# Optimization experiments

Measured on AMD Instinct MI355X. Metric: run time of the kernel, lower is better.

Reference implementation:

```python
import jax, jax.numpy as jnp
import numpy as np

B, L, D, H, F, NL, K, G = 2, 2048, 768, 12, 3072, 12, 128, 16
HD = D // H
SCALE = HD ** -0.5


def setup_inputs() -> dict:
    key = jax.random.key(0)
    ks = jax.random.split(key, 8)
    n = lambda k, s, std=0.02: jax.random.normal(k, s, dtype=jnp.float32) * std
    return {
        "x": jax.random.normal(ks[0], (B, L, D), dtype=jnp.float32),
        "pos_conv_w": n(ks[1], (D, D // G, K)),
        "pos_conv_b": jnp.zeros((D,), jnp.float32),
        "ln0_g": jnp.ones((D,), jnp.float32), "ln0_b": jnp.zeros((D,), jnp.float32),
        "Wq": n(ks[2], (NL, D, D)), "bq": jnp.zeros((NL, D), jnp.float32),
        "Wk": n(ks[3], (NL, D, D)), "bk": jnp.zeros((NL, D), jnp.float32),
        "Wv": n(ks[4], (NL, D, D)), "bv": jnp.zeros((NL, D), jnp.float32),
        "Wo": n(ks[5], (NL, D, D)), "bo": jnp.zeros((NL, D), jnp.float32),
        "ln1_g": jnp.ones((NL, D), jnp.float32), "ln1_b": jnp.zeros((NL, D), jnp.float32),
        "W1": n(ks[6], (NL, D, F)), "b1": jnp.zeros((NL, F), jnp.float32),
        "W2": n(ks[7], (NL, F, D)), "b2": jnp.zeros((NL, D), jnp.float32),
        "ln2_g": jnp.ones((NL, D), jnp.float32), "ln2_b": jnp.zeros((NL, D), jnp.float32),
    }


def _ln(x, g, b, eps=1e-5):
    m = jnp.mean(x, axis=-1, keepdims=True)
    v = jnp.mean(jnp.square(x - m), axis=-1, keepdims=True)
    return (x - m) * jax.lax.rsqrt(v + eps) * g + b


def reference(x, pos_conv_w, pos_conv_b, ln0_g, ln0_b, Wq, bq, Wk, bk, Wv, bv, Wo, bo,
              ln1_g, ln1_b, W1, b1, W2, b2, ln2_g, ln2_b):
    b_, l_, d_ = x.shape
    # positional grouped conv embedding (kernel even -> drop last frame), GELU, residual add
    pos = jax.lax.conv_general_dilated(x.transpose(0, 2, 1), pos_conv_w, (1,), [(K // 2, K // 2)],
                                       feature_group_count=G)  # (B, D, L+1)
    pos = pos[:, :, :l_] + pos_conv_b[None, :, None]
    h = x + jax.nn.gelu(pos, approximate=False).transpose(0, 2, 1)
    # post-norm encoder (layer_norm_first=False): LN applied before the layer stack
    h = _ln(h, ln0_g, ln0_b)

    def layer(h, p):
        wq, bq_, wk, bk_, wv, bv_, wo, bo_, g1, be1, w1, bf1, w2, bf2, g2, be2 = p
        r = h
        q = (h @ wq + bq_).reshape(b_, l_, H, HD)
        k = (h @ wk + bk_).reshape(b_, l_, H, HD)
        v = (h @ wv + bv_).reshape(b_, l_, H, HD)
        w = jax.nn.softmax(SCALE * jnp.einsum('blhd,bmhd->bhlm', q, k), axis=-1)
        o = jnp.einsum('bhlm,bmhd->blhd', w, v).reshape(b_, l_, d_)
        h = r + (o @ wo + bo_)
        h = _ln(h, g1, be1)
        ff = jax.nn.gelu(h @ w1 + bf1, approximate=False) @ w2 + bf2
        h = _ln(h + ff, g2, be2)
        return h, None

    h, _ = jax.lax.scan(layer, h, (Wq, bq, Wk, bk, Wv, bv, Wo, bo,
                                   ln1_g, ln1_b, W1, b1, W2, b2, ln2_g, ln2_b))
    return h
```

## Files before the change

kernel.cpp:

```cpp
#include <hip/hip_runtime.h>
#include <hip/hip_bf16.h>
#include <stdint.h>

#define B_ 2
#define L_ 2048
#define D_ 768
#define H_ 12
#define F_ 3072
#define NL_ 12
#define K_ 128
#define G_ 16
#define HD_ 64
#define CPG_ 48
#define M_TOK (B_*L_)
#define SCALE_ 0.125f

typedef __hip_bfloat16 bf16;
typedef __bf16 bf16x8 __attribute__((ext_vector_type(8)));
typedef float f32x4 __attribute__((ext_vector_type(4)));

__device__ __forceinline__ void gload16(const void* g, void* l) {
  __builtin_amdgcn_global_load_lds((const __attribute__((address_space(1))) void*)g,
                                   (__attribute__((address_space(3))) void*)l, 16, 0, 0);
}

__global__ __launch_bounds__(256) void convw_kernel(const float* __restrict__ w,
                                                    bf16* __restrict__ wT2) {
  int idx = blockIdx.x * 256 + threadIdx.x;
  int ci = idx & 63;
  int row = idx >> 6;
  int d = row % 48;
  int t2 = row / 48;
  int kk = t2 & 127;
  int g = t2 >> 7;
  float v = (ci < 48) ? w[(((size_t)(g * 48 + d) * 48) + ci) * 128 + kk] : 0.f;
  wT2[idx] = __float2bfloat16(v);
}

__global__ __launch_bounds__(256) void conv_mfma(const float* __restrict__ x,
                                                 const bf16* __restrict__ wT2,
                                                 const float* __restrict__ bias,
                                                 float* __restrict__ out) {
  int flat = blockIdx.x;
  int wgid = (flat & 7) * 64 + (flat >> 3);
  const int g = wgid >> 5;
  int rem = wgid & 31;
  const int l0 = (rem & 15) * 128;
  const int b = rem >> 4;

  const int tid = threadIdx.x, w = tid >> 6, lane = tid & 63;
  const int c15 = lane & 15, g4 = lane >> 4;
  __shared__ __align__(16) bf16 win[256 * 64];
  __shared__ __align__(16) bf16 Wl[2][2 * 48 * 64];

  {
    int lg = l0 - 64 + tid;
    char* dst = (char*)win + tid * 128;
    int swr = (tid & 7) << 4;
    uint4 z4 = {0u, 0u, 0u, 0u};
    if ((unsigned)lg < 2048u) {
      const float* srow = x + ((size_t)(b * 2048 + lg) * 768 + g * 48);
#pragma unroll
      for (int c = 0; c < 6; ++c) {
        float4 v0 = *(const float4*)(srow + c * 8);
        float4 v1 = *(const float4*)(srow + c * 8 + 4);
        union { bf16 h[8]; uint4 u; } uu;
        uu.h[0] = __float2bfloat16(v0.x); uu.h[1] = __float2bfloat16(v0.y);
        uu.h[2] = __float2bfloat16(v0.z); uu.h[3] = __float2bfloat16(v0.w);
        uu.h[4] = __float2bfloat16(v1.x); uu.h[5] = __float2bfloat16(v1.y);
        uu.h[6] = __float2bfloat16(v1.z); uu.h[7] = __float2bfloat16(v1.w);
        *(uint4*)(dst + ((c * 16) ^ swr)) = uu.u;
      }
    } else {
#pragma unroll
      for (int c = 0; c < 6; ++c) *(uint4*)(dst + ((c * 16) ^ swr)) = z4;
    }
    *(uint4*)(dst + (96 ^ swr)) = z4;
    *(uint4*)(dst + (112 ^ swr)) = z4;
  }

  const char* wbase = (const char*)wT2 + (size_t)g * 128 * 48 * 128;

  const int coff = w * 3072;
#define STAGEW(kp, bufi)                                                                   \
  {                                                                                        \
    _Pragma("unroll")                                                                      \
    for (int i = 0; i < 3; ++i) {                                                          \
      int c = coff + i * 1024 + (lane << 4);                                               \
      int row96 = c >> 7;                                                                  \
      int s = row96 / 48;                                                                  \
      int d = row96 - s * 48;                                                              \
      int cb2 = c & 127;                                                                   \
      gload16(wbase + ((size_t)((2 * (kp) + s) * 48 + d)) * 128 + (cb2 ^ ((d & 7) << 4)),  \
              (char*)Wl[bufi] + coff + i * 1024);                                          \
    }                                                                                      \
  }

  f32x4 acc[2][3];
  const f32x4 vzero = {0.f, 0.f, 0.f, 0.f};
#pragma unroll
  for (int i = 0; i < 2; ++i)
#pragma unroll
    for (int j = 0; j < 3; ++j) acc[i][j] = vzero;

  STAGEW(0, 0);
  __syncthreads();

  for (int kp = 0; kp < 64; ++kp) {
    int cur = kp & 1;
    if (kp + 1 < 64) STAGEW(kp + 1, cur ^ 1);
    const char* Wc = (const char*)Wl[cur];
#pragma unroll
    for (int s = 0; s < 2; ++s) {
      int kk = 2 * kp + s;
#pragma unroll
      for (int cb = 0; cb < 2; ++cb) {
        int a0r = w * 16 + c15 + kk;
        int a1r = 64 + a0r;
        bf16x8 a0 = *(const bf16x8*)((const char*)win + a0r * 128 + ((cb * 64 + g4 * 16) ^ ((a0r & 7) << 4)));
        bf16x8 a1 = *(const bf16x8*)((const char*)win + a1r * 128 + ((cb * 64 + g4 * 16) ^ ((a1r & 7) << 4)));
#pragma unroll
        for (int ct = 0; ct < 3; ++ct) {
          int d = ct * 16 + c15;
          bf16x8 bfrag = *(const bf16x8*)(Wc + s * 6144 + d * 128 +
                                          ((cb * 64 + g4 * 16) ^ ((d & 7) << 4)));
          acc[0][ct] = __builtin_amdgcn_mfma_f32_16x16x32_bf16(a0, bfrag, acc[0][ct], 0, 0, 0);
          acc[1][ct] = __builtin_amdgcn_mfma_f32_16x16x32_bf16(a1, bfrag, acc[1][ct], 0, 0, 0);
        }
      }
    }
    __syncthreads();
  }
#undef STAGEW

#pragma unroll
  for (int ls = 0; ls < 2; ++ls)
#pragma unroll
    for (int ct = 0; ct < 3; ++ct) {
      int dg = g * 48 + ct * 16 + c15;
      float bv = bias[dg];
#pragma unroll
      for (int r = 0; r < 4; ++r) {
        int l = l0 + ls * 64 + w * 16 + g4 * 4 + r;
        size_t idx = (size_t)(b * 2048 + l) * 768 + dg;
        float vv = acc[ls][ct][r] + bv;
        vv = 0.5f * vv * (1.0f + erff(vv * 0.70710678f));
        out[idx] = x[idx] + vv;
      }
    }
}

__global__ __launch_bounds__(256) void ln_kernel(const float* __restrict__ a,
                                                 const float* __restrict__ g,
                                                 const float* __restrict__ be,
                                                 bf16* __restrict__ outb) {
  int w = threadIdx.x >> 6, lane = threadIdx.x & 63;
  size_t row = (size_t)blockIdx.x * 4 + w;
  const float* ar = a + row * 768;
  float4 v[3];
  float s = 0.f;
#pragma unroll
  for (int i = 0; i < 3; ++i) {
    int c = lane * 4 + i * 256;
    float4 vv = *(const float4*)(ar + c);
    v[i] = vv;
    s += vv.x + vv.y + vv.z + vv.w;
  }
#pragma unroll
  for (int st = 1; st < 64; st <<= 1) s += __shfl_xor(s, st);
  float mean = s * (1.0f / 768.0f);
  float s2 = 0.f;
#pragma unroll
  for (int i = 0; i < 3; ++i) {
    float dx = v[i].x - mean, dy = v[i].y - mean, dz = v[i].z - mean, dw = v[i].w - mean;
    s2 += dx * dx + dy * dy + dz * dz + dw * dw;
  }
#pragma unroll
  for (int st = 1; st < 64; st <<= 1) s2 += __shfl_xor(s2, st);
  float rstd = rsqrtf(s2 * (1.0f / 768.0f) + 1e-5f);
#pragma unroll
  for (int i = 0; i < 3; ++i) {
    int c = lane * 4 + i * 256;
    float4 gv = *(const float4*)(g + c);
    float4 bv = *(const float4*)(be + c);
    union { bf16 h[4]; uint2 u; } pk;
    pk.h[0] = __float2bfloat16((v[i].x - mean) * rstd * gv.x + bv.x);
    pk.h[1] = __float2bfloat16((v[i].y - mean) * rstd * gv.y + bv.y);
    pk.h[2] = __float2bfloat16((v[i].z - mean) * rstd * gv.z + bv.z);
    pk.h[3] = __float2bfloat16((v[i].w - mean) * rstd * gv.w + bv.w);
    *(uint2*)(outb + row * 768 + c) = pk.u;
  }
}

template <int F32OUT>
__global__ __launch_bounds__(256) void ln_bf(const bf16* __restrict__ a,
                                             const bf16* __restrict__ r,
                                             const float* __restrict__ g,
                                             const float* __restrict__ be,
                                             bf16* __restrict__ outb,
                                             float* __restrict__ outf) {
  int w = threadIdx.x >> 6, lane = threadIdx.x & 63;
  size_t row = (size_t)blockIdx.x * 4 + w;
  const bf16* ar = a + row * 768;
  const bf16* rr = r + row * 768;
  float v[3][4];
  float s = 0.f;
#pragma unroll
  for (int i = 0; i < 3; ++i) {
    int c = lane * 4 + i * 256;
    union { uint2 u; uint16_t h[4]; } ua, urr;
    ua.u = *(const uint2*)(ar + c);
    urr.u = *(const uint2*)(rr + c);
#pragma unroll
    for (int j = 0; j < 4; ++j) {
      float x = __uint_as_float((uint32_t)ua.h[j] << 16) +
                __uint_as_float((uint32_t)urr.h[j] << 16);
      v[i][j] = x; s += x;
    }
  }
#pragma unroll
  for (int st = 1; st < 64; st <<= 1) s += __shfl_xor(s, st);
  float mean = s * (1.0f / 768.0f);
  float s2 = 0.f;
#pragma unroll
  for (int i = 0; i < 3; ++i)
#pragma unroll
    for (int j = 0; j < 4; ++j) {
      float d2 = v[i][j] - mean;
      s2 += d2 * d2;
    }
#pragma unroll
  for (int st = 1; st < 64; st <<= 1) s2 += __shfl_xor(s2, st);
  float rstd = rsqrtf(s2 * (1.0f / 768.0f) + 1e-5f);
#pragma unroll
  for (int i = 0; i < 3; ++i) {
    int c = lane * 4 + i * 256;
    float4 gv = *(const float4*)(g + c);
    float4 bv = *(const float4*)(be + c);
    float o0 = (v[i][0] - mean) * rstd * gv.x + bv.x;
    float o1 = (v[i][1] - mean) * rstd * gv.y + bv.y;
    float o2 = (v[i][2] - mean) * rstd * gv.z + bv.z;
    float o3 = (v[i][3] - mean) * rstd * gv.w + bv.w;
    union { bf16 h[4]; uint2 u; } pk;
    pk.h[0] = __float2bfloat16(o0); pk.h[1] = __float2bfloat16(o1);
    pk.h[2] = __float2bfloat16(o2); pk.h[3] = __float2bfloat16(o3);
    *(uint2*)(outb + row * 768 + c) = pk.u;
    if (F32OUT) {
      float4 of = {o0, o1, o2, o3};
      *(float4*)(outf + row * 768 + c) = of;
    }
  }
}

__global__ __launch_bounds__(256) void prep_weights(const float* __restrict__ WqB,
                                                    const float* __restrict__ WkB,
                                                    const float* __restrict__ WvB,
                                                    const float* __restrict__ WoB,
                                                    const float* __restrict__ W1B,
                                                    const float* __restrict__ W2B,
                                                    const float* __restrict__ bqB,
                                                    const float* __restrict__ bkB,
                                                    const float* __restrict__ bvB,
                                                    bf16* __restrict__ wqkvb,
                                                    bf16* __restrict__ wob,
                                                    bf16* __restrict__ w1b,
                                                    bf16* __restrict__ w2b,
                                                    float* __restrict__ bqkv,
                                                    int l) {
  __shared__ float t[32][33];
  int tid = threadIdx.x;
  int tx = tid & 31, ty = tid >> 5;
  const float* wq = WqB + (size_t)l * 768 * 768;
  const float* wk = WkB + (size_t)l * 768 * 768;
  const float* wv = WvB + (size_t)l * 768 * 768;
  const float* wo = WoB + (size_t)l * 768 * 768;
  const float* w1 = W1B + (size_t)l * 768 * 3072;
  const float* w2 = W2B + (size_t)l * 3072 * 768;

  int blk = blockIdx.x;
  if (blk >= 6912) {
    int i = (blk - 6912) * 256 + tid;
    if (i < 2304)
      bqkv[i] = (i < 768) ? bqB[(size_t)l * 768 + i]
              : (i < 1536) ? bkB[(size_t)l * 768 + i - 768]
                           : bvB[(size_t)l * 768 + i - 1536];
    return;
  }
  if (blk < 1728) {
    int n0 = (blk % 72) * 32, k0 = (blk / 72) * 32;
    const float* src = (n0 < 768) ? wq : (n0 < 1536) ? wk : wv;
    int nn = (n0 >= 1536) ? (n0 - 1536) : (n0 >= 768 ? n0 - 768 : n0);
#pragma unroll
    for (int i = 0; i < 32; i += 8) t[ty + i][tx] = src[(size_t)(k0 + ty + i) * 768 + nn + tx];
    __syncthreads();
#pragma unroll
    for (int i = 0; i < 32; i += 8)
      wqkvb[(size_t)(n0 + ty + i) * 768 + k0 + tx] = __float2bfloat16(t[tx][ty + i]);
    return;
  }
  blk -= 1728;
  if (blk < 576) {
    int c0 = (blk % 24) * 32, r0 = (blk / 24) * 32;
#pragma unroll
    for (int i = 0; i < 32; i += 8) t[ty + i][tx] = wo[(size_t)(r0 + ty + i) * 768 + c0 + tx];
    __syncthreads();
#pragma unroll
    for (int i = 0; i < 32; i += 8)
      wob[(size_t)(c0 + ty + i) * 768 + r0 + tx] = __float2bfloat16(t[tx][ty + i]);
    return;
  }
  blk -= 576;
  if (blk < 2304) {
    int c0 = (blk % 96) * 32, r0 = (blk / 96) * 32;
#pragma unroll
    for (int i = 0; i < 32; i += 8) t[ty + i][tx] = w1[(size_t)(r0 + ty + i) * 3072 + c0 + tx];
    __syncthreads();
#pragma unroll
    for (int i = 0; i < 32; i += 8)
      w1b[(size_t)(c0 + ty + i) * 768 + r0 + tx] = __float2bfloat16(t[tx][ty + i]);
    return;
  }
  blk -= 2304;
  {
    int c0 = (blk % 24) * 32, r0 = (blk / 24) * 32;
#pragma unroll
    for (int i = 0; i < 32; i += 8) t[ty + i][tx] = w2[(size_t)(r0 + ty + i) * 768 + c0 + tx];
    __syncthreads();
#pragma unroll
    for (int i = 0; i < 32; i += 8)
      w2b[(size_t)(c0 + ty + i) * 3072 + r0 + tx] = __float2bfloat16(t[tx][ty + i]);
  }
}

template <int BM, int BN, int BK, int GELU, int BF16OUT, int VOUT = 0>
__global__ __launch_bounds__(256) void gemm_bf16(const bf16* __restrict__ A,
                                                 const bf16* __restrict__ BT,
                                                 const float* __restrict__ bias,
                                                 void* __restrict__ Cout,
                                                 int N, int Kd,
                                                 bf16* __restrict__ vTout = nullptr) {
  constexpr int WM = BM / 2, MF = WM / 16;
  constexpr int WN = BN / 2, FN = WN / 16;
  constexpr int KF = BK / 32;
  constexpr int ROWB = BK * 2;
  constexpr int RPC = 1024 / ROWB;
  constexpr int NCH = BM * BK / 512;
  __shared__ bf16 As[BM * BK];
  __shared__ bf16 Bs[BN * BK];
  const int tid = threadIdx.x, w = tid >> 6, lane = tid & 63;
  int gx = gridDim.x;
  int flat = blockIdx.x + gx * blockIdx.y;
  int cpx = (gx * gridDim.y) >> 3;
  int sw = (flat & 7) * cpx + (flat >> 3);
  const int bn = sw % gx, bm = sw / gx;
  const int wr = w >> 1, wc = w & 1;
  const int c15 = lane & 15, g4 = lane >> 4;
  const int rowInC = lane / (ROWB / 16);
  const int colb = (lane % (ROWB / 16)) * 16;

  f32x4 acc[MF][FN];
  const f32x4 vzero = {0.f, 0.f, 0.f, 0.f};
#pragma unroll
  for (int i = 0; i < MF; ++i)
#pragma unroll
    for (int j = 0; j < FN; ++j) acc[i][j] = vzero;

  const char* Ab = (const char*)A;
  const char* Bb = (const char*)BT;

  for (int k0 = 0; k0 < Kd; k0 += BK) {
#pragma unroll
    for (int i = 0; i < NCH / 4; ++i) {
      int t = w + 4 * i;
      int row = t * RPC + rowInC;
      gload16(Ab + ((size_t)(bm * BM + row) * Kd + k0) * 2 + (colb ^ ((row & 7) << 4)),
              (char*)As + t * 1024);
    }
#pragma unroll
    for (int i = 0; i < (BN * BK / 512) / 4; ++i) {
      int t = w + 4 * i;
      int row = t * RPC + rowInC;
      gload16(Bb + ((size_t)(bn * BN + row) * Kd + k0) * 2 + (colb ^ ((row & 7) << 4)),
              (char*)Bs + t * 1024);
    }
    __syncthreads();
    bf16x8 af[MF][KF], bfr[FN][KF];
#pragma unroll
    for (int kf = 0; kf < KF; ++kf) {
      int kbyte = kf * 64 + g4 * 16;
#pragma unroll
      for (int mf = 0; mf < MF; ++mf) {
        int row = wr * WM + mf * 16 + c15;
        af[mf][kf] = *(const bf16x8*)((const char*)As + row * ROWB + (kbyte ^ ((row & 7) << 4)));
      }
#pragma unroll
      for (int fn = 0; fn < FN; ++fn) {
        int row = wc * WN + fn * 16 + c15;
        bfr[fn][kf] = *(const bf16x8*)((const char*)Bs + row * ROWB + (kbyte ^ ((row & 7) << 4)));
      }
    }
    __builtin_amdgcn_s_setprio(1);
#pragma unroll
    for (int mf = 0; mf < MF; ++mf)
#pragma unroll
      for (int fn = 0; fn < FN; ++fn)
#pragma unroll
        for (int kf = 0; kf < KF; ++kf)
          acc[mf][fn] = __builtin_amdgcn_mfma_f32_16x16x32_bf16(af[mf][kf], bfr[fn][kf], acc[mf][fn], 0, 0, 0);
    __builtin_amdgcn_s_setprio(0);
    __syncthreads();
  }
#pragma unroll
  for (int fn = 0; fn < FN; ++fn) {
    int col = bn * BN + wc * WN + fn * 16 + c15;
    float bv = bias[col];
#pragma unroll
    for (int mf = 0; mf < MF; ++mf) {
#pragma unroll
      for (int r = 0; r < 4; ++r) {
        int row = bm * BM + wr * WM + mf * 16 + g4 * 4 + r;
        float vv = acc[mf][fn][r] + bv;
        if (GELU) vv = 0.5f * vv * (1.0f + erff(vv * 0.70710678f));
        if (BF16OUT) {
          if (VOUT && col >= 1536) {
            int hd2 = col - 1536, hh = hd2 >> 6, dd = hd2 & 63;
            int bb = row >> 11, ll = row & 2047;
            vTout[((size_t)((bb * 12 + hh) * 64 + dd) << 11) + ll] = __float2bfloat16(vv);
          } else {
            ((bf16*)Cout)[(size_t)row * N + col] = __float2bfloat16(vv);
          }
        } else {
          ((float*)Cout)[(size_t)row * N + col] = vv;
        }
      }
    }
  }
}

__global__ __launch_bounds__(256) void attn_mfma(const bf16* __restrict__ qkv,
                                                 const bf16* __restrict__ vT,
                                                 bf16* __restrict__ ob) {
  int bid = blockIdx.x + 32 * (blockIdx.y + 12 * blockIdx.z);
  int wgid = (bid & 7) * 96 + (bid >> 3);
  const int q0 = (wgid & 31) * 64;
  int bh = wgid >> 5;
  const int h = bh % 12, b = bh / 12;

  const int tid = threadIdx.x, w = tid >> 6, lane = tid & 63;
  const int c15 = lane & 15, g4 = lane >> 4;
  const int lrow8 = lane >> 3;
  const int cb = (lane & 7) * 16;
  __shared__ bf16 Kl[2][4096];
  __shared__ bf16 Vl[2][4096];
  __shared__ bf16 Pl[4096];

  const f32x4 vzero = {0.f, 0.f, 0.f, 0.f};
  const char* qp = (const char*)qkv + (((size_t)(b * 2048 + q0 + w * 16 + c15)) * 2304 + h * 64) * 2;
  bf16x8 qa0 = *(const bf16x8*)(qp + g4 * 16);
  bf16x8 qa1 = *(const bf16x8*)(qp + 64 + g4 * 16);

  bf16x8 b_one;
#pragma unroll
  for (int i = 0; i < 8; ++i) b_one[i] = (__bf16)1.0f;

  f32x4 o[4], o5;
#pragma unroll
  for (int i = 0; i < 4; ++i) o[i] = vzero;
  o5 = vzero;
  float m = -1e30f;
  const float SC2 = 0.18033688f;
  const float THR = 11.54f;

  const char* kgb = (const char*)qkv + (((size_t)(b * 2048)) * 2304 + 768 + h * 64) * 2;
  const char* vgb = (const char*)vT + ((size_t)((b * 12 + h) * 64) * 2048) * 2;
  char* Plw = (char*)Pl + w * 2048;

  const int rr0 = w * 8 + lrow8;
  const int swz = cb ^ (lrow8 << 4);
  const char* ka0 = kgb + (size_t)rr0 * 4608 + swz;
  const char* ka1 = ka0 + 32 * 4608;
  const char* va0 = vgb + (size_t)rr0 * 4096 + swz;
  const char* va1 = va0 + 32 * 4096;
  char* kd0 = (char*)Kl[0] + w * 1024;
  char* vd0 = (char*)Vl[0] + w * 1024;

#define STAGE(kt, bufi)                                                        \
  {                                                                            \
    size_t ko = (size_t)(kt) * 294912;                                         \
    size_t vo = (size_t)(kt) * 128;                                            \
    int lo = (bufi) * 8192;                                                    \
    gload16(ka0 + ko, kd0 + lo);                                               \
    gload16(ka1 + ko, kd0 + lo + 4096);                                        \
    gload16(va0 + vo, vd0 + lo);                                               \
    gload16(va1 + vo, vd0 + lo + 4096);                                        \
  }

  STAGE(0, 0);
  __syncthreads();

  for (int kt = 0; kt < 32; ++kt) {
    int cur = kt & 1;
    if (kt + 1 < 32) STAGE(kt + 1, cur ^ 1);

    const char* Kc = (const char*)Kl[cur];
    const char* Vc = (const char*)Vl[cur];

    f32x4 sc[4];
    __builtin_amdgcn_s_setprio(1);
#pragma unroll
    for (int fn = 0; fn < 4; ++fn) {
      int key = fn * 16 + c15;
      const char* kr = Kc + key * 128;
      int sw = (key & 7) << 4;
      bf16x8 kb0 = *(const bf16x8*)(kr + ((g4 * 16) ^ sw));
      bf16x8 kb1 = *(const bf16x8*)(kr + ((64 + g4 * 16) ^ sw));
      f32x4 s = __builtin_amdgcn_mfma_f32_16x16x32_bf16(kb0, qa0, vzero, 0, 0, 0);
      s = __builtin_amdgcn_mfma_f32_16x16x32_bf16(kb1, qa1, s, 0, 0, 0);
      sc[fn] = s;
    }
    __builtin_amdgcn_s_setprio(0);

    float pm = fmaxf(
        fmaxf(fmaxf(fmaxf(sc[0][0], sc[0][1]), fmaxf(sc[0][2], sc[0][3])),
              fmaxf(fmaxf(sc[1][0], sc[1][1]), fmaxf(sc[1][2], sc[1][3]))),
        fmaxf(fmaxf(fmaxf(sc[2][0], sc[2][1]), fmaxf(sc[2][2], sc[2][3])),
              fmaxf(fmaxf(sc[3][0], sc[3][1]), fmaxf(sc[3][2], sc[3][3]))));
    int ok = (pm * SC2 <= m + THR) ? 1 : 0;

    if (!__all(ok)) {
      float tm = pm;
      tm = fmaxf(tm, __shfl_xor(tm, 16));
      tm = fmaxf(tm, __shfl_xor(tm, 32));
      float mn = fmaxf(m, tm * SC2);
      float alpha = exp2f(m - mn);
      m = mn;
#pragma unroll
      for (int r = 0; r < 4; ++r) {
        float ar = __shfl(alpha, g4 * 4 + r);
        o[0][r] *= ar; o[1][r] *= ar; o[2][r] *= ar; o[3][r] *= ar;
        o5[r] *= ar;
      }
    }

    {
      char* prow = Plw + c15 * 128;
      int swp = (c15 & 7) << 4;
#pragma unroll
      for (int fn = 0; fn < 4; ++fn) {
        union { bf16 hh[4]; uint2 u; } pk;
#pragma unroll
        for (int r = 0; r < 4; ++r)
          pk.hh[r] = __float2bfloat16(exp2f(fmaf(sc[fn][r], SC2, -m)));
        *(uint2*)(prow + ((fn * 32 + g4 * 8) ^ swp)) = pk.u;
      }
    }

    {
      const char* pr = Plw + c15 * 128;
      int sw = (c15 & 7) << 4;
      bf16x8 pa0 = *(const bf16x8*)(pr + ((g4 * 16) ^ sw));
      bf16x8 pa1 = *(const bf16x8*)(pr + ((64 + g4 * 16) ^ sw));
      __builtin_amdgcn_s_setprio(1);
#pragma unroll
      for (int fh = 0; fh < 4; ++fh) {
        int hd = fh * 16 + c15;
        const char* vr = Vc + hd * 128;
        int swv = (hd & 7) << 4;
        bf16x8 vb0 = *(const bf16x8*)(vr + ((g4 * 16) ^ swv));
        bf16x8 vb1 = *(const bf16x8*)(vr + ((64 + g4 * 16) ^ swv));
        o[fh] = __builtin_amdgcn_mfma_f32_16x16x32_bf16(pa0, vb0, o[fh], 0, 0, 0);
        o[fh] = __builtin_amdgcn_mfma_f32_16x16x32_bf16(pa1, vb1, o[fh], 0, 0, 0);
      }
      o5 = __builtin_amdgcn_mfma_f32_16x16x32_bf16(pa0, b_one, o5, 0, 0, 0);
      o5 = __builtin_amdgcn_mfma_f32_16x16x32_bf16(pa1, b_one, o5, 0, 0, 0);
      __builtin_amdgcn_s_setprio(0);
    }
    __syncthreads();
  }
#undef STAGE

#pragma unroll
  for (int r = 0; r < 4; ++r) {
    float inv = 1.0f / o5[r];
    size_t row = (size_t)(b * 2048 + q0 + w * 16 + g4 * 4 + r);
#pragma unroll
    for (int fh = 0; fh < 4; ++fh)
      ob[row * 768 + h * 64 + fh * 16 + c15] = __float2bfloat16(o[fh][r] * inv);
  }
}

extern "C" void kernel_launch(void* const* d_in, const int* in_sizes, int n_in,
                              void* d_out, int out_size, void* d_ws, size_t ws_size,
                              hipStream_t stream) {
  const float* x      = (const float*)d_in[0];
  const float* pcw    = (const float*)d_in[1];
  const float* pcb    = (const float*)d_in[2];
  const float* ln0_g  = (const float*)d_in[3];
  const float* ln0_b  = (const float*)d_in[4];
  const float* Wq     = (const float*)d_in[5];
  const float* bq     = (const float*)d_in[6];
  const float* Wk     = (const float*)d_in[7];
  const float* bk     = (const float*)d_in[8];
  const float* Wv     = (const float*)d_in[9];
  const float* bv     = (const float*)d_in[10];
  const float* Wo     = (const float*)d_in[11];
  const float* bo     = (const float*)d_in[12];
  const float* ln1_g  = (const float*)d_in[13];
  const float* ln1_b  = (const float*)d_in[14];
  const float* W1     = (const float*)d_in[15];
  const float* b1     = (const float*)d_in[16];
  const float* W2     = (const float*)d_in[17];
  const float* b2     = (const float*)d_in[18];
  const float* ln2_g  = (const float*)d_in[19];
  const float* ln2_b  = (const float*)d_in[20];

  const size_t MDB = (size_t)M_TOK * D_ * 4;
  char* W = (char*)d_ws;
  float* tmp  = (float*)(W + MDB);
  char*  big  = W + 2 * MDB;
  bf16*  qkv  = (bf16*)big;
  bf16*  ff   = (bf16*)big;
  bf16*  wT2  = (bf16*)big;
  bf16*  tmp_bf = (bf16*)W;
  char* p = W + 2 * MDB + 25165824;
  bf16* h_bf  = (bf16*)p; p += (size_t)M_TOK * D_ * 2;
  bf16* obuf  = (bf16*)p; p += (size_t)M_TOK * D_ * 2;
  bf16* vT    = (bf16*)p; p += (size_t)M_TOK * D_ * 2;
  bf16* wqkvb = (bf16*)p; p += (size_t)2304 * 768 * 2;
  bf16* wob   = (bf16*)p; p += (size_t)768 * 768 * 2;
  bf16* w1b   = (bf16*)p; p += (size_t)3072 * 768 * 2;
  bf16* w2b   = (bf16*)p; p += (size_t)768 * 3072 * 2;
  float* bqkv = (float*)p;

  convw_kernel<<<24576, 256, 0, stream>>>(pcw, wT2);
  conv_mfma<<<512, 256, 0, stream>>>(x, wT2, pcb, tmp);
  ln_kernel<<<M_TOK / 4, 256, 0, stream>>>(tmp, ln0_g, ln0_b, h_bf);

  for (int l = 0; l < NL_; ++l) {
    prep_weights<<<6921, 256, 0, stream>>>(Wq, Wk, Wv, Wo, W1, W2, bq, bk, bv,
                                           wqkvb, wob, w1b, w2b, bqkv, l);

    gemm_bf16<128, 128, 64, 0, 1, 1><<<dim3(18, 32), 256, 0, stream>>>(h_bf, wqkvb, bqkv, qkv, 2304, 768, vT);
    attn_mfma<<<dim3(32, 12, 2), 256, 0, stream>>>(qkv, vT, obuf);
    gemm_bf16<64, 64, 128, 0, 1><<<dim3(12, 64), 256, 0, stream>>>(obuf, wob, bo + (size_t)l * D_, tmp_bf, 768, 768);
    ln_bf<0><<<M_TOK / 4, 256, 0, stream>>>(tmp_bf, h_bf, ln1_g + (size_t)l * D_, ln1_b + (size_t)l * D_, h_bf, nullptr);
    gemm_bf16<128, 128, 64, 1, 1><<<dim3(24, 32), 256, 0, stream>>>(h_bf, w1b, b1 + (size_t)l * F_, ff, 3072, 768);
    gemm_bf16<64, 64, 128, 0, 1><<<dim3(12, 64), 256, 0, stream>>>(ff, w2b, b2 + (size_t)l * D_, tmp_bf, 768, 3072);
    if (l == NL_ - 1)
      ln_bf<1><<<M_TOK / 4, 256, 0, stream>>>(tmp_bf, h_bf, ln2_g + (size_t)l * D_, ln2_b + (size_t)l * D_, h_bf, (float*)d_out);
    else
      ln_bf<0><<<M_TOK / 4, 256, 0, stream>>>(tmp_bf, h_bf, ln2_g + (size_t)l * D_, ln2_b + (size_t)l * D_, h_bf, nullptr);
  }
}
```

Measured before the change: 2.256 ms.

## Software-pipeline attention: compute next QK tile before current softmax and PV

Restructures the flash-attention main loop so the QK^T MFMAs for tile kt+1 are issued before the softmax and PV work for tile kt, using two score register sets. K and V loads are split and prefetched two tiles ahead, with V moved to a triple-buffered LDS array. The goal is to overlap MFMA work with the exp/max softmax math and with global-to-LDS load latency. The cost is more register pressure and LDS, which could lower occupancy. The barrier-driven vmcnt waits may also limit how much overlap is actually achieved.

```diff
diff --git a/kernel.cpp b/kernel.cpp
--- a/kernel.cpp
+++ b/kernel.cpp
@@ -80,7 +80,6 @@
   }
 
   const char* wbase = (const char*)wT2 + (size_t)g * 128 * 48 * 128;
-
   const int coff = w * 3072;
 #define STAGEW(kp, bufi)                                                                   \
   {                                                                                        \
@@ -451,7 +450,7 @@
   const int lrow8 = lane >> 3;
   const int cb = (lane & 7) * 16;
   __shared__ bf16 Kl[2][4096];
-  __shared__ bf16 Vl[2][4096];
+  __shared__ bf16 Vl[3][4096];
   __shared__ bf16 Pl[4096];
 
   const f32x4 vzero = {0.f, 0.f, 0.f, 0.f};
@@ -484,100 +483,123 @@
   char* kd0 = (char*)Kl[0] + w * 1024;
   char* vd0 = (char*)Vl[0] + w * 1024;
 
-#define STAGE(kt, bufi)                                                        \
+#define STAGE_K(kt, bufi)                                                      \
   {                                                                            \
     size_t ko = (size_t)(kt) * 294912;                                         \
-    size_t vo = (size_t)(kt) * 128;                                            \
     int lo = (bufi) * 8192;                                                    \
     gload16(ka0 + ko, kd0 + lo);                                               \
     gload16(ka1 + ko, kd0 + lo + 4096);                                        \
+  }
+#define STAGE_V(kt, bufi)                                                      \
+  {                                                                            \
+    size_t vo = (size_t)(kt) * 128;                                            \
+    int lo = (bufi) * 8192;                                                    \
     gload16(va0 + vo, vd0 + lo);                                               \
     gload16(va1 + vo, vd0 + lo + 4096);                                        \
   }
 
-  STAGE(0, 0);
+#define DO_QK(SC, kbuf)                                                        \
+  {                                                                            \
+    const char* Kc = (const char*)Kl[kbuf];                                    \
+    __builtin_amdgcn_s_setprio(1);                                             \
+    _Pragma("unroll")                                                          \
+    for (int fn = 0; fn < 4; ++fn) {                                           \
+      int key = fn * 16 + c15;                                                 \
+      const char* kr = Kc + key * 128;                                         \
+      int swk = (key & 7) << 4;                                                \
+      bf16x8 kb0 = *(const bf16x8*)(kr + ((g4 * 16) ^ swk));                   \
+      bf16x8 kb1 = *(const bf16x8*)(kr + ((64 + g4 * 16) ^ swk));              \
+      f32x4 s = __builtin_amdgcn_mfma_f32_16x16x32_bf16(kb0, qa0, vzero, 0, 0, 0); \
+      s = __builtin_amdgcn_mfma_f32_16x16x32_bf16(kb1, qa1, s, 0, 0, 0);       \
+      SC[fn] = s;                                                              \
+    }                                                                          \
+    __builtin_amdgcn_s_setprio(0);                                             \
+  }
+
+#define DO_SMPV(SC, vbuf)                                                      \
+  {                                                                            \
+    float pm = fmaxf(                                                          \
+        fmaxf(fmaxf(fmaxf(SC[0][0], SC[0][1]), fmaxf(SC[0][2], SC[0][3])),     \
+              fmaxf(fmaxf(SC[1][0], SC[1][1]), fmaxf(SC[1][2], SC[1][3]))),    \
+        fmaxf(fmaxf(fmaxf(SC[2][0], SC[2][1]), fmaxf(SC[2][2], SC[2][3])),     \
+              fmaxf(fmaxf(SC[3][0], SC[3][1]), fmaxf(SC[3][2], SC[3][3]))));   \
+    int ok = (pm * SC2 <= m + THR) ? 1 : 0;                                    \
+    if (!__all(ok)) {                                                          \
+      float tm = pm;                                                           \
+      tm = fmaxf(tm, __shfl_xor(tm, 16));                                      \
+      tm = fmaxf(tm, __shfl_xor(tm, 32));                                      \
+      float mn = fmaxf(m, tm * SC2);                                           \
+      float alpha = exp2f(m - mn);                                             \
+      m = mn;                                                                  \
+      _Pragma("unroll")                                                        \
+      for (int r = 0; r < 4; ++r) {                                            \
+        float ar = __shfl(alpha, g4 * 4 + r);                                  \
+        o[0][r] *= ar; o[1][r] *= ar; o[2][r] *= ar; o[3][r] *= ar;            \
+        o5[r] *= ar;                                                           \
+      }                                                                        \
+    }                                                                          \
+    {                                                                          \
+      char* prow = Plw + c15 * 128;                                            \
+      int swp = (c15 & 7) << 4;                                                \
+      _Pragma("unroll")                                                        \
+      for (int fn = 0; fn < 4; ++fn) {                                         \
+        union { bf16 hh[4]; uint2 u; } pk;                                     \
+        _Pragma("unroll")                                                      \
+        for (int r = 0; r < 4; ++r)                                            \
+          pk.hh[r] = __float2bfloat16(exp2f(fmaf(SC[fn][r], SC2, -m)));        \
+        *(uint2*)(prow + ((fn * 32 + g4 * 8) ^ swp)) = pk.u;                   \
+      }                                                                        \
+    }                                                                          \
+    {                                                                          \
+      const char* pr = Plw + c15 * 128;                                        \
+      int swp2 = (c15 & 7) << 4;                                               \
+      bf16x8 pa0 = *(const bf16x8*)(pr + ((g4 * 16) ^ swp2));                  \
+      bf16x8 pa1 = *(const bf16x8*)(pr + ((64 + g4 * 16) ^ swp2));             \
+      const char* Vc = (const char*)Vl[vbuf];                                  \
+      __builtin_amdgcn_s_setprio(1);                                           \
+      _Pragma("unroll")                                                        \
+      for (int fh = 0; fh < 4; ++fh) {                                         \
+        int hd = fh * 16 + c15;                                                \
+        const char* vr = Vc + hd * 128;                                        \
+        int swv = (hd & 7) << 4;                                               \
+        bf16x8 vb0 = *(const bf16x8*)(vr + ((g4 * 16) ^ swv));                 \
+        bf16x8 vb1 = *(const bf16x8*)(vr + ((64 + g4 * 16) ^ swv));            \
+        o[fh] = __builtin_amdgcn_mfma_f32_16x16x32_bf16(pa0, vb0, o[fh], 0, 0, 0); \
+        o[fh] = __builtin_amdgcn_mfma_f32_16x16x32_bf16(pa1, vb1, o[fh], 0, 0, 0); \
+      }                                                                        \
+      o5 = __builtin_amdgcn_mfma_f32_16x16x32_bf16(pa0, b_one, o5, 0, 0, 0);   \
+      o5 = __builtin_amdgcn_mfma_f32_16x16x32_bf16(pa1, b_one, o5, 0, 0, 0);   \
+      __builtin_amdgcn_s_setprio(0);                                           \
+    }                                                                          \
+  }
+
+  STAGE_K(0, 0); STAGE_K(1, 1); STAGE_V(0, 0); STAGE_V(1, 1);
   __syncthreads();
 
-  for (int kt = 0; kt < 32; ++kt) {
-    int cur = kt & 1;
-    if (kt + 1 < 32) STAGE(kt + 1, cur ^ 1);
-
-    const char* Kc = (const char*)Kl[cur];
-    const char* Vc = (const char*)Vl[cur];
-
-    f32x4 sc[4];
-    __builtin_amdgcn_s_setprio(1);
-#pragma unroll
-    for (int fn = 0; fn < 4; ++fn) {
-      int key = fn * 16 + c15;
-      const char* kr = Kc + key * 128;
-      int sw = (key & 7) << 4;
-      bf16x8 kb0 = *(const bf16x8*)(kr + ((g4 * 16) ^ sw));
-      bf16x8 kb1 = *(const bf16x8*)(kr + ((64 + g4 * 16) ^ sw));
-      f32x4 s = __builtin_amdgcn_mfma_f32_16x16x32_bf16(kb0, qa0, vzero, 0, 0, 0);
-      s = __builtin_amdgcn_mfma_f32_16x16x32_bf16(kb1, qa1, s, 0, 0, 0);
-      sc[fn] = s;
-    }
-    __builtin_amdgcn_s_setprio(0);
-
-    float pm = fmaxf(
-        fmaxf(fmaxf(fmaxf(sc[0][0], sc[0][1]), fmaxf(sc[0][2], sc[0][3])),
-              fmaxf(fmaxf(sc[1][0], sc[1][1]), fmaxf(sc[1][2], sc[1][3]))),
-        fmaxf(fmaxf(fmaxf(sc[2][0], sc[2][1]), fmaxf(sc[2][2], sc[2][3])),
-              fmaxf(fmaxf(sc[3][0], sc[3][1]), fmaxf(sc[3][2], sc[3][3]))));
-    int ok = (pm * SC2 <= m + THR) ? 1 : 0;
-
-    if (!__all(ok)) {
-      float tm = pm;
-      tm = fmaxf(tm, __shfl_xor(tm, 16));
-      tm = fmaxf(tm, __shfl_xor(tm, 32));
-      float mn = fmaxf(m, tm * SC2);
-      float alpha = exp2f(m - mn);
-      m = mn;
-#pragma unroll
-      for (int r = 0; r < 4; ++r) {
-        float ar = __shfl(alpha, g4 * 4 + r);
-        o[0][r] *= ar; o[1][r] *= ar; o[2][r] *= ar; o[3][r] *= ar;
-        o5[r] *= ar;
-      }
-    }
-
-    {
-      char* prow = Plw + c15 * 128;
-      int swp = (c15 & 7) << 4;
-#pragma unroll
-      for (int fn = 0; fn < 4; ++fn) {
-        union { bf16 hh[4]; uint2 u; } pk;
-#pragma unroll
-        for (int r = 0; r < 4; ++r)
-          pk.hh[r] = __float2bfloat16(exp2f(fmaf(sc[fn][r], SC2, -m)));
-        *(uint2*)(prow + ((fn * 32 + g4 * 8) ^ swp)) = pk.u;
-      }
-    }
-
-    {
-      const char* pr = Plw + c15 * 128;
-      int sw = (c15 & 7) << 4;
-      bf16x8 pa0 = *(const bf16x8*)(pr + ((g4 * 16) ^ sw));
-      bf16x8 pa1 = *(const bf16x8*)(pr + ((64 + g4 * 16) ^ sw));
-      __builtin_amdgcn_s_setprio(1);
-#pragma unroll
-      for (int fh = 0; fh < 4; ++fh) {
-        int hd = fh * 16 + c15;
-        const char* vr = Vc + hd * 128;
-        int swv = (hd & 7) << 4;
-        bf16x8 vb0 = *(const bf16x8*)(vr + ((g4 * 16) ^ swv));
-        bf16x8 vb1 = *(const bf16x8*)(vr + ((64 + g4 * 16) ^ swv));
-        o[fh] = __builtin_amdgcn_mfma_f32_16x16x32_bf16(pa0, vb0, o[fh], 0, 0, 0);
-        o[fh] = __builtin_amdgcn_mfma_f32_16x16x32_bf16(pa1, vb1, o[fh], 0, 0, 0);
-      }
-      o5 = __builtin_amdgcn_mfma_f32_16x16x32_bf16(pa0, b_one, o5, 0, 0, 0);
-      o5 = __builtin_amdgcn_mfma_f32_16x16x32_bf16(pa1, b_one, o5, 0, 0, 0);
-      __builtin_amdgcn_s_setprio(0);
-    }
-    __syncthreads();
-  }
-#undef STAGE
+  f32x4 scA[4], scB[4];
+  DO_QK(scA, 0);
+
+#define ITER(kt, SCUR, SNXT)                                                   \
+  {                                                                            \
+    if ((kt) + 2 < 32) {                                                       \
+      STAGE_K((kt) + 2, (kt) & 1);                                             \
+      STAGE_V((kt) + 2, ((kt) + 2) % 3);                                       \
+    }                                                                          \
+    if ((kt) + 1 < 32) DO_QK(SNXT, ((kt) + 1) & 1);                            \
+    DO_SMPV(SCUR, (kt) % 3);                                                   \
+    __syncthreads();                                                           \
+  }
+
+#pragma unroll 2
+  for (int kt2 = 0; kt2 < 32; kt2 += 2) {
+    ITER(kt2, scA, scB);
+    ITER(kt2 + 1, scB, scA);
+  }
+#undef ITER
+#undef DO_SMPV
+#undef DO_QK
+#undef STAGE_K
+#undef STAGE_V
 
 #pragma unroll
   for (int r = 0; r < 4; ++r) {
```

Measured after the change: 2.236 ms, median of 2. Within noise of the previous version (-0.9%).
